# Optimization experiments

Hardware: AMD Instinct MI355X
Metric: run time of the kernel (lower is better)

The kernel has to match this reference:

```python
import jax, jax.numpy as jnp
import numpy as np

NUM_EMBEDDINGS = 128
EMBEDDING_DIM = 256
COMMITMENT_COST = 0.25
B, T = 64, 2048


def setup_inputs() -> dict:
    key = jax.random.key(0)
    k1, k2 = jax.random.split(key)
    inputs = jax.random.normal(k1, (B, T, EMBEDDING_DIM), dtype=jnp.float32)
    # codebook initialized like nn.Embedding weight (uniform in torch, normal fine for baseline)
    embedding = jax.random.normal(k2, (NUM_EMBEDDINGS, EMBEDDING_DIM), dtype=jnp.float32)
    return {"inputs": inputs, "embedding": embedding}


def reference(inputs, embedding):
    # eval-mode VectorQuantizerEMA.forward
    input_shape = inputs.shape
    flat = inputs.reshape(-1, EMBEDDING_DIM)                      # [N, D]
    distances = (
        jnp.sum(flat * flat, axis=1, keepdims=True)
        + jnp.sum(embedding * embedding, axis=1)
        - 2.0 * jnp.matmul(flat, embedding.T)
    )
    encoding_indices = jnp.argmin(distances, axis=1)              # [N]
    encodings = jax.nn.one_hot(encoding_indices, NUM_EMBEDDINGS, dtype=inputs.dtype)  # [N, K]
    quantized = embedding[encoding_indices].reshape(input_shape)  # gather lookup

    e_latent_loss = jnp.mean((jax.lax.stop_gradient(quantized) - inputs) ** 2)
    loss = COMMITMENT_COST * e_latent_loss

    # straight-through estimator
    quantized_st = inputs + jax.lax.stop_gradient(quantized - inputs)

    avg_probs = jnp.mean(encodings, axis=0)
    perplexity = jnp.exp(-jnp.sum(avg_probs * jnp.log(avg_probs + 1e-10)))

    encoding_indices = encoding_indices.reshape(input_shape[0], input_shape[1])
    return (loss, quantized_st, perplexity, encodings, encoding_indices)
```

## Files before the change

kernel.cpp:

```cpp
#include <hip/hip_runtime.h>
#include <math.h>

#define NUM_K 128
#define DIM   256
#define NROWS (64 * 2048)
#define BLOCK 256
#define RPB   128
#define GRID  (NROWS / RPB)

#define OFF_LOSS 0u
#define OFF_Q    1u
#define OFF_PERP 33554433u
#define OFF_ENC  33554434u
#define OFF_IDX  50331650u


typedef __attribute__((ext_vector_type(8))) short bf16x8;
typedef __attribute__((ext_vector_type(4))) float f32x4;
typedef float f4a __attribute__((ext_vector_type(4), aligned(4)));

union PackU { uint4 u; bf16x8 v; };

__device__ __forceinline__ bf16x8 pack_hi16(const unsigned int* w) {
  PackU p;
  p.u.x = (w[1] & 0xFFFF0000u) | (w[0] >> 16);
  p.u.y = (w[3] & 0xFFFF0000u) | (w[2] >> 16);
  p.u.z = (w[5] & 0xFFFF0000u) | (w[4] >> 16);
  p.u.w = (w[7] & 0xFFFF0000u) | (w[6] >> 16);
  return p.v;
}

__device__ __forceinline__ void split3(const float* xf, bf16x8& a, bf16x8& b, bf16x8& c) {
  unsigned int ua[8], ub[8], uc[8];
  #pragma unroll
  for (int i = 0; i < 8; ++i) {
    float x = xf[i];
    unsigned int ha = __float_as_uint(x) & 0xFFFF0000u;
    float r1 = x - __uint_as_float(ha);
    unsigned int hb = __float_as_uint(r1) & 0xFFFF0000u;
    float r2 = r1 - __uint_as_float(hb);
    ua[i] = ha; ub[i] = hb; uc[i] = __float_as_uint(r2);
  }
  a = pack_hi16(ua); b = pack_hi16(ub); c = pack_hi16(uc);
}

__global__ void vq_init(const float* __restrict__ E, float* __restrict__ ws) {
    int k = blockIdx.x, lane = threadIdx.x;
    float4 v = *(const float4*)(E + (size_t)k * DIM + lane * 4);
    float s = v.x * v.x + v.y * v.y + v.z * v.z + v.w * v.w;
    #pragma unroll
    for (int off = 32; off; off >>= 1) s += __shfl_down(s, off);
    if (lane == 0) ws[256 + k] = s;
    if (k == 0) {
        if (lane == 0) ws[0] = 0.0f;
        ((int*)ws)[64 + lane]  = 0;
        ((int*)ws)[128 + lane] = 0;
    }
}

__global__ __launch_bounds__(BLOCK, 2) void vq_main(
        const float* __restrict__ X, const float* __restrict__ E,
        float* ws, float* __restrict__ out) {
    const int tid  = threadIdx.x;
    const int lane = tid & 63;
    const int kg   = __builtin_amdgcn_readfirstlane(tid >> 6);
    const int l4   = lane & 15;
    const int g    = lane >> 4;
    const int r0   = blockIdx.x * RPB;

    __shared__ float rd[4][RPB];
    __shared__ int   ri[4][RPB];
    __shared__ int   idxs[RPB];
    __shared__ int   hcnt[NUM_K];
    if (tid < NUM_K) hcnt[tid] = 0;

    const float* xp = X + (size_t)(r0 + l4) * DIM + g * 8;
    const float* ep = E + (size_t)(kg * 32 + l4) * DIM + g * 8;

    f32x4 acc[8][2];
    #pragma unroll
    for (int rt = 0; rt < 8; ++rt) {
        acc[rt][0] = (f32x4)0.0f;
        acc[rt][1] = (f32x4)0.0f;
    }
    float sx = 0.0f;

    #pragma unroll 1
    for (int half = 0; half < 2; ++half) {
        const int kbase = half * 128;
        bf16x8 ea[2][4], eb[2][4], ec[2][4];
        #pragma unroll
        for (int ct = 0; ct < 2; ++ct) {
            #pragma unroll
            for (int ch = 0; ch < 4; ++ch) {
                const float* p = ep + (size_t)ct * 16 * DIM + kbase + ch * 32;
                float4 v0 = *(const float4*)(p);
                float4 v1 = *(const float4*)(p + 4);
                float xf[8] = {v0.x, v0.y, v0.z, v0.w, v1.x, v1.y, v1.z, v1.w};
                split3(xf, ea[ct][ch], eb[ct][ch], ec[ct][ch]);
            }
        }
        #pragma unroll
        for (int rt = 0; rt < 8; ++rt) {
            #pragma unroll
            for (int ch = 0; ch < 4; ++ch) {
                const float* p = xp + (size_t)rt * 16 * DIM + kbase + ch * 32;
                float4 v0 = *(const float4*)(p);
                float4 v1 = *(const float4*)(p + 4);
                float xf[8] = {v0.x, v0.y, v0.z, v0.w, v1.x, v1.y, v1.z, v1.w};
                if (kg == 0) {
                    #pragma unroll
                    for (int i = 0; i < 8; ++i) sx = fmaf(xf[i], xf[i], sx);
                }
                bf16x8 xa, xb, xc;
                split3(xf, xa, xb, xc);
                acc[rt][0] = __builtin_amdgcn_mfma_f32_16x16x32_bf16(xa, ea[0][ch], acc[rt][0], 0, 0, 0);
                acc[rt][1] = __builtin_amdgcn_mfma_f32_16x16x32_bf16(xa, ea[1][ch], acc[rt][1], 0, 0, 0);
                acc[rt][0] = __builtin_amdgcn_mfma_f32_16x16x32_bf16(xa, eb[0][ch], acc[rt][0], 0, 0, 0);
                acc[rt][1] = __builtin_amdgcn_mfma_f32_16x16x32_bf16(xa, eb[1][ch], acc[rt][1], 0, 0, 0);
                acc[rt][0] = __builtin_amdgcn_mfma_f32_16x16x32_bf16(xb, ea[0][ch], acc[rt][0], 0, 0, 0);
                acc[rt][1] = __builtin_amdgcn_mfma_f32_16x16x32_bf16(xb, ea[1][ch], acc[rt][1], 0, 0, 0);
                acc[rt][0] = __builtin_amdgcn_mfma_f32_16x16x32_bf16(xa, ec[0][ch], acc[rt][0], 0, 0, 0);
                acc[rt][1] = __builtin_amdgcn_mfma_f32_16x16x32_bf16(xa, ec[1][ch], acc[rt][1], 0, 0, 0);
                acc[rt][0] = __builtin_amdgcn_mfma_f32_16x16x32_bf16(xc, ea[0][ch], acc[rt][0], 0, 0, 0);
                acc[rt][1] = __builtin_amdgcn_mfma_f32_16x16x32_bf16(xc, ea[1][ch], acc[rt][1], 0, 0, 0);
                acc[rt][0] = __builtin_amdgcn_mfma_f32_16x16x32_bf16(xb, eb[0][ch], acc[rt][0], 0, 0, 0);
                acc[rt][1] = __builtin_amdgcn_mfma_f32_16x16x32_bf16(xb, eb[1][ch], acc[rt][1], 0, 0, 0);
            }
        }
        __syncthreads();
    }

    const float* sep = ws + 256 + kg * 32;
    const float se0 = sep[l4];
    const float se1 = sep[l4 + 16];
    const int   c0  = kg * 32 + l4;

    #pragma unroll
    for (int rt = 0; rt < 8; ++rt) {
        #pragma unroll
        for (int r = 0; r < 4; ++r) {
            float t0 = fmaf(-2.0f, acc[rt][0][r], se0);
            float t1 = fmaf(-2.0f, acc[rt][1][r], se1);
            float t; int ci;
            if (t1 < t0) { t = t1; ci = c0 + 16; } else { t = t0; ci = c0; }
            #pragma unroll
            for (int m = 1; m <= 8; m <<= 1) {
                float tv = __shfl_xor(t, m);
                int   cv = __shfl_xor(ci, m);
                if (tv < t || (tv == t && cv < ci)) { t = tv; ci = cv; }
            }
            if (l4 == 0) {
                int rl = rt * 16 + g * 4 + r;
                rd[kg][rl] = t;
                ri[kg][rl] = ci;
            }
        }
    }

    if (kg == 0) {
        #pragma unroll
        for (int m = 1; m <= 32; m <<= 1) sx += __shfl_xor(sx, m);
        if (lane == 0) atomicAdd(&ws[0], sx);
    }
    __syncthreads();

    if (tid < RPB) {
        float dm = rd[0][tid]; int ix = ri[0][tid];
        #pragma unroll
        for (int gg = 1; gg < 4; ++gg) {
            float t = rd[gg][tid];
            if (t < dm) { dm = t; ix = ri[gg][tid]; }
        }
        idxs[tid] = ix;
        out[OFF_IDX + r0 + tid] = (float)ix;
        atomicAdd(&hcnt[ix], 1);
        float v = dm;
        #pragma unroll
        for (int m = 1; m <= 32; m <<= 1) v += __shfl_xor(v, m);
        if ((tid & 63) == 0) atomicAdd(&ws[0], v);
    }
    __syncthreads();
    if (tid < NUM_K && hcnt[tid]) atomicAdd((int*)ws + 64 + tid, hcnt[tid]);

    #pragma unroll 4
    for (int it = 0; it < 32; ++it) {
        int r  = it * 4 + (tid >> 6);
        int ix = idxs[r];
        float4 v = *(const float4*)(E + (size_t)ix * DIM + (tid & 63) * 4);
        f4a w = {v.x, v.y, v.z, v.w};
        *(f4a*)(out + OFF_Q + (size_t)(r0 + r) * DIM + (tid & 63) * 4) = w;
    }
    #pragma unroll 4
    for (int it = 0; it < 16; ++it) {
        int s  = it * BLOCK + tid;
        int r  = s >> 5;
        int c4 = (s & 31) * 4;
        int ix = idxs[r];
        f4a e4;
        e4.x = (c4     == ix) ? 1.0f : 0.0f;
        e4.y = (c4 + 1 == ix) ? 1.0f : 0.0f;
        e4.z = (c4 + 2 == ix) ? 1.0f : 0.0f;
        e4.w = (c4 + 3 == ix) ? 1.0f : 0.0f;
        *(f4a*)(out + OFF_ENC + (size_t)(r0 + r) * NUM_K + c4) = e4;
    }
}

__global__ void vq_final(const float* __restrict__ ws, float* __restrict__ out) {
    int t = threadIdx.x;
    if (t == 0) out[OFF_LOSS] = 0.25f * (ws[0] / (float)((size_t)NROWS * DIM));
    int c = ((const int*)ws)[64 + t];
    float p = (float)c / (float)NROWS;
    float v = p * logf(p + 1e-10f);
    #pragma unroll
    for (int off = 32; off; off >>= 1) v += __shfl_down(v, off);
    __shared__ float red[2];
    if ((t & 63) == 0) red[t >> 6] = v;
    __syncthreads();
    if (t == 0) out[OFF_PERP] = expf(-(red[0] + red[1]));
}

extern "C" void kernel_launch(void* const* d_in, const int* in_sizes, int n_in,
                              void* d_out, int out_size, void* d_ws, size_t ws_size,
                              hipStream_t stream) {
    const float* X = (const float*)d_in[0];
    const float* E = (const float*)d_in[1];
    float* out = (float*)d_out;
    float* ws  = (float*)d_ws;

    vq_init <<<NUM_K, 64, 0, stream>>>(E, ws);
    vq_main <<<GRID, BLOCK, 0, stream>>>(X, E, ws, out);
    vq_final<<<1, 128, 0, stream>>>(ws, out);
}
```

Measured before the change: 423.2 us.

## Precompute codebook bf16 splits once and retile main kernel over 64 rows

Adds a pre-pass kernel that splits the codebook into three bf16 parts once and stores them in workspace, so the main kernel no longer re-splits E in every block. The main kernel is retiled to 64 rows per block, with waves split into two row halves and two code halves. It loads X chunk by chunk with software prefetch of the next chunk, and launch bounds rise to 3 blocks per CU. The old kernel is kept as a fallback when the workspace is too small, which adds code paths and relies on the workspace size at run time.

```diff
diff --git a/kernel.cpp b/kernel.cpp
--- a/kernel.cpp
+++ b/kernel.cpp
@@ -5,8 +5,11 @@
 #define DIM   256
 #define NROWS (64 * 2048)
 #define BLOCK 256
-#define RPB   128
+
+#define RPB   64
 #define GRID  (NROWS / RPB)
+#define RPB_F 128
+#define GRID_F (NROWS / RPB_F)
 
 #define OFF_LOSS 0u
 #define OFF_Q    1u
@@ -14,6 +17,8 @@
 #define OFF_ENC  33554434u
 #define OFF_IDX  50331650u
 
+#define WS_EF_FLOATS 512
+#define WS_NEEDED    (WS_EF_FLOATS * 4 + 64 * 3 * 64 * 16)
 
 typedef __attribute__((ext_vector_type(8))) short bf16x8;
 typedef __attribute__((ext_vector_type(4))) float f32x4;
@@ -58,7 +63,178 @@
     }
 }
 
-__global__ __launch_bounds__(BLOCK, 2) void vq_main(
+__global__ void vq_esplit(const float* __restrict__ E, float* __restrict__ ws) {
+    int b = blockIdx.x, lane = threadIdx.x;
+    int code = (b & 7) * 16 + (lane & 15);
+    int d0   = (b >> 3) * 32 + (lane >> 4) * 8;
+    const float* p = E + (size_t)code * DIM + d0;
+    float4 v0 = *(const float4*)(p);
+    float4 v1 = *(const float4*)(p + 4);
+    float xf[8] = {v0.x, v0.y, v0.z, v0.w, v1.x, v1.y, v1.z, v1.w};
+    bf16x8 a, bq, c;
+    split3(xf, a, bq, c);
+    bf16x8* dst = (bf16x8*)(ws + WS_EF_FLOATS);
+    dst[(b * 3 + 0) * 64 + lane] = a;
+    dst[(b * 3 + 1) * 64 + lane] = bq;
+    dst[(b * 3 + 2) * 64 + lane] = c;
+}
+
+__global__ __launch_bounds__(BLOCK, 3) void vq_main(
+        const float* __restrict__ X, const float* __restrict__ E,
+        float* ws, float* __restrict__ out) {
+    const int tid  = threadIdx.x;
+    const int lane = tid & 63;
+    const int kg   = __builtin_amdgcn_readfirstlane(tid >> 6);
+    const int pr   = kg & 1;
+    const int rh   = kg >> 1;
+    const int l4   = lane & 15;
+    const int g    = lane >> 4;
+    const int r0   = blockIdx.x * RPB;
+
+    __shared__ float rd[2][RPB];
+    __shared__ int   ri[2][RPB];
+    __shared__ int   idxs[RPB];
+    __shared__ int   hcnt[NUM_K];
+    if (tid < NUM_K) hcnt[tid] = 0;
+
+    const float* xb = X + (size_t)(r0 + rh * 32 + l4) * DIM + g * 8;
+    const bf16x8* __restrict__ EF = (const bf16x8*)(ws + WS_EF_FLOATS);
+
+    f32x4 acc[2][4];
+    #pragma unroll
+    for (int rt = 0; rt < 2; ++rt)
+        #pragma unroll
+        for (int ct = 0; ct < 4; ++ct) acc[rt][ct] = (f32x4)0.0f;
+    float sx = 0.0f;
+
+    float4 a00 = *(const float4*)(xb);
+    float4 a01 = *(const float4*)(xb + 4);
+    float4 a10 = *(const float4*)(xb + 16 * DIM);
+    float4 a11 = *(const float4*)(xb + 16 * DIM + 4);
+
+    #pragma unroll
+    for (int ch = 0; ch < 8; ++ch) {
+        bf16x8 ef[4][3];
+        #pragma unroll
+        for (int ct = 0; ct < 4; ++ct) {
+            const int CB = (ch * 8 + pr * 4 + ct) * 3;
+            #pragma unroll
+            for (int s = 0; s < 3; ++s) ef[ct][s] = EF[(CB + s) * 64 + lane];
+        }
+        float4 c00 = a00, c01 = a01, c10 = a10, c11 = a11;
+        if (ch < 7) {
+            const float* nx = xb + (ch + 1) * 32;
+            a00 = *(const float4*)(nx);
+            a01 = *(const float4*)(nx + 4);
+            a10 = *(const float4*)(nx + 16 * DIM);
+            a11 = *(const float4*)(nx + 16 * DIM + 4);
+        }
+        float x0[8] = {c00.x, c00.y, c00.z, c00.w, c01.x, c01.y, c01.z, c01.w};
+        float x1[8] = {c10.x, c10.y, c10.z, c10.w, c11.x, c11.y, c11.z, c11.w};
+        if (pr == 0) {
+            #pragma unroll
+            for (int i = 0; i < 8; ++i) {
+                sx = fmaf(x0[i], x0[i], sx);
+                sx = fmaf(x1[i], x1[i], sx);
+            }
+        }
+        bf16x8 xa0, xb0, xc0, xa1, xb1, xc1;
+        split3(x0, xa0, xb0, xc0);
+        split3(x1, xa1, xb1, xc1);
+#define MF(XP0, XP1, ES)                                                      \
+        _Pragma("unroll")                                                     \
+        for (int ct = 0; ct < 4; ++ct) {                                      \
+            acc[0][ct] = __builtin_amdgcn_mfma_f32_16x16x32_bf16(XP0, ef[ct][ES], acc[0][ct], 0, 0, 0); \
+            acc[1][ct] = __builtin_amdgcn_mfma_f32_16x16x32_bf16(XP1, ef[ct][ES], acc[1][ct], 0, 0, 0); \
+        }
+        MF(xa0, xa1, 0)
+        MF(xa0, xa1, 1)
+        MF(xb0, xb1, 0)
+        MF(xa0, xa1, 2)
+        MF(xc0, xc1, 0)
+        MF(xb0, xb1, 1)
+#undef MF
+    }
+
+    const float* sep = ws + 256 + pr * 64;
+    const float se0 = sep[l4];
+    const float se1 = sep[l4 + 16];
+    const float se2 = sep[l4 + 32];
+    const float se3 = sep[l4 + 48];
+    const int   cb  = pr * 64 + l4;
+
+    #pragma unroll
+    for (int rt = 0; rt < 2; ++rt) {
+        #pragma unroll
+        for (int r = 0; r < 4; ++r) {
+            float t0 = fmaf(-2.0f, acc[rt][0][r], se0);
+            float t1 = fmaf(-2.0f, acc[rt][1][r], se1);
+            float t2 = fmaf(-2.0f, acc[rt][2][r], se2);
+            float t3 = fmaf(-2.0f, acc[rt][3][r], se3);
+            float t = t0; int ci = cb;
+            if (t1 < t) { t = t1; ci = cb + 16; }
+            if (t2 < t) { t = t2; ci = cb + 32; }
+            if (t3 < t) { t = t3; ci = cb + 48; }
+            #pragma unroll
+            for (int m = 1; m <= 8; m <<= 1) {
+                float tv = __shfl_xor(t, m);
+                int   cv = __shfl_xor(ci, m);
+                if (tv < t || (tv == t && cv < ci)) { t = tv; ci = cv; }
+            }
+            if (l4 == 0) {
+                int rl = rh * 32 + rt * 16 + g * 4 + r;
+                rd[pr][rl] = t;
+                ri[pr][rl] = ci;
+            }
+        }
+    }
+
+    if (pr == 0) {
+        #pragma unroll
+        for (int m = 1; m <= 32; m <<= 1) sx += __shfl_xor(sx, m);
+        if (lane == 0) atomicAdd(&ws[0], sx);
+    }
+    __syncthreads();
+
+    if (tid < RPB) {
+        float dm = rd[0][tid]; int ix = ri[0][tid];
+        float t  = rd[1][tid];
+        if (t < dm) { dm = t; ix = ri[1][tid]; }
+        idxs[tid] = ix;
+        out[OFF_IDX + r0 + tid] = (float)ix;
+        atomicAdd(&hcnt[ix], 1);
+        float v = dm;
+        #pragma unroll
+        for (int m = 1; m <= 32; m <<= 1) v += __shfl_xor(v, m);
+        if (tid == 0) atomicAdd(&ws[0], v);
+    }
+    __syncthreads();
+    if (tid < NUM_K && hcnt[tid]) atomicAdd((int*)ws + 64 + tid, hcnt[tid]);
+
+    #pragma unroll 4
+    for (int it = 0; it < 16; ++it) {
+        int r  = it * 4 + (tid >> 6);
+        int ix = idxs[r];
+        float4 v = *(const float4*)(E + (size_t)ix * DIM + (tid & 63) * 4);
+        f4a w = {v.x, v.y, v.z, v.w};
+        *(f4a*)(out + OFF_Q + (size_t)(r0 + r) * DIM + (tid & 63) * 4) = w;
+    }
+    #pragma unroll 4
+    for (int it = 0; it < 8; ++it) {
+        int s  = it * BLOCK + tid;
+        int r  = s >> 5;
+        int c4 = (s & 31) * 4;
+        int ix = idxs[r];
+        f4a e4;
+        e4.x = (c4     == ix) ? 1.0f : 0.0f;
+        e4.y = (c4 + 1 == ix) ? 1.0f : 0.0f;
+        e4.z = (c4 + 2 == ix) ? 1.0f : 0.0f;
+        e4.w = (c4 + 3 == ix) ? 1.0f : 0.0f;
+        *(f4a*)(out + OFF_ENC + (size_t)(r0 + r) * NUM_K + c4) = e4;
+    }
+}
+
+__global__ __launch_bounds__(BLOCK, 2) void vq_main_f(
         const float* __restrict__ X, const float* __restrict__ E,
         float* ws, float* __restrict__ out) {
     const int tid  = threadIdx.x;
@@ -66,11 +242,11 @@
     const int kg   = __builtin_amdgcn_readfirstlane(tid >> 6);
     const int l4   = lane & 15;
     const int g    = lane >> 4;
-    const int r0   = blockIdx.x * RPB;
-
-    __shared__ float rd[4][RPB];
-    __shared__ int   ri[4][RPB];
-    __shared__ int   idxs[RPB];
+    const int r0   = blockIdx.x * RPB_F;
+
+    __shared__ float rd[4][RPB_F];
+    __shared__ int   ri[4][RPB_F];
+    __shared__ int   idxs[RPB_F];
     __shared__ int   hcnt[NUM_K];
     if (tid < NUM_K) hcnt[tid] = 0;
 
@@ -79,10 +255,7 @@
 
     f32x4 acc[8][2];
     #pragma unroll
-    for (int rt = 0; rt < 8; ++rt) {
-        acc[rt][0] = (f32x4)0.0f;
-        acc[rt][1] = (f32x4)0.0f;
-    }
+    for (int rt = 0; rt < 8; ++rt) { acc[rt][0] = (f32x4)0.0f; acc[rt][1] = (f32x4)0.0f; }
     float sx = 0.0f;
 
     #pragma unroll 1
@@ -165,7 +338,7 @@
     }
     __syncthreads();
 
-    if (tid < RPB) {
+    if (tid < RPB_F) {
         float dm = rd[0][tid]; int ix = ri[0][tid];
         #pragma unroll
         for (int gg = 1; gg < 4; ++gg) {
@@ -228,7 +401,12 @@
     float* out = (float*)d_out;
     float* ws  = (float*)d_ws;
 
-    vq_init <<<NUM_K, 64, 0, stream>>>(E, ws);
-    vq_main <<<GRID, BLOCK, 0, stream>>>(X, E, ws, out);
+    vq_init<<<NUM_K, 64, 0, stream>>>(E, ws);
+    if (ws_size >= (size_t)WS_NEEDED) {
+        vq_esplit<<<64, 64, 0, stream>>>(E, ws);
+        vq_main  <<<GRID, BLOCK, 0, stream>>>(X, E, ws, out);
+    } else {
+        vq_main_f<<<GRID_F, BLOCK, 0, stream>>>(X, E, ws, out);
+    }
     vq_final<<<1, 128, 0, stream>>>(ws, out);
 }
```

Result: faster. 358.8 us (-15.2%).
